# Optimization experiments

Measured on AMD Instinct MI355X. Metric: run time of the kernel, lower is better.

## Reference

```python
import jax, jax.numpy as jnp
import numpy as np

B, S, HID = 2, 2048, 2304
H, KVH, D = 8, 4, 256          # query heads, kv heads, head_dim
N_REP = H // KVH
SCALE = 256.0 ** -0.5          # query_pre_attn_scalar ** -0.5
SOFTCAP = 50.0
ROPE_THETA = 10000.0
NEG = -1e9


def setup_inputs() -> dict:
    key = jax.random.key(0)
    k1, k2, k3, k4, k5 = jax.random.split(key, 5)
    hidden_states = jax.random.normal(k1, (B, S, HID), dtype=jnp.float32)
    # RoPE cos/sin tables, shape [B, S, D]
    inv_freq = 1.0 / (ROPE_THETA ** (jnp.arange(0, D, 2, dtype=jnp.float32) / D))
    pos = jnp.arange(S, dtype=jnp.float32)
    freqs = pos[:, None] * inv_freq[None, :]            # [S, D/2]
    emb = jnp.concatenate([freqs, freqs], axis=-1)      # [S, D]
    cos = jnp.broadcast_to(jnp.cos(emb)[None], (B, S, D))
    sin = jnp.broadcast_to(jnp.sin(emb)[None], (B, S, D))
    # additive causal mask [B, 1, S, S] (sliding_window=4096 > S, so pure causal)
    idx = jnp.arange(S)
    causal = idx[None, :] <= idx[:, None]
    attention_mask = jnp.broadcast_to(
        jnp.where(causal, 0.0, NEG).astype(jnp.float32)[None, None], (B, 1, S, S))
    # projection weights (lecun-normal-ish scale), no bias (attention_bias=False)
    Wq = jax.random.normal(k2, (HID, H * D), dtype=jnp.float32) / np.sqrt(HID)
    Wk = jax.random.normal(k3, (HID, KVH * D), dtype=jnp.float32) / np.sqrt(HID)
    Wv = jax.random.normal(k4, (HID, KVH * D), dtype=jnp.float32) / np.sqrt(HID)
    Wo = jax.random.normal(k5, (H * D, HID), dtype=jnp.float32) / np.sqrt(H * D)
    return {"hidden_states": hidden_states, "cos": cos, "sin": sin,
            "attention_mask": attention_mask,
            "Wq": Wq, "Wk": Wk, "Wv": Wv, "Wo": Wo}


def _rotate_half(x):
    half = x.shape[-1] // 2
    return jnp.concatenate([-x[..., half:], x[..., :half]], axis=-1)


def reference(hidden_states, cos, sin, attention_mask, Wq, Wk, Wv, Wo):
    b, s, _ = hidden_states.shape
    q = (hidden_states @ Wq).reshape(b, s, H, D).transpose(0, 2, 1, 3)    # [B,H,S,D]
    k = (hidden_states @ Wk).reshape(b, s, KVH, D).transpose(0, 2, 1, 3)  # [B,KVH,S,D]
    v = (hidden_states @ Wv).reshape(b, s, KVH, D).transpose(0, 2, 1, 3)
    c = cos[:, None]  # [B,1,S,D] broadcast over heads (unsqueeze_dim=1)
    sn = sin[:, None]
    q = q * c + _rotate_half(q) * sn
    k = k * c + _rotate_half(k) * sn
    # GQA: repeat kv heads (interleave, matching repeat_kv tile+reshape)
    k = jnp.repeat(k, N_REP, axis=1)
    v = jnp.repeat(v, N_REP, axis=1)
    w = jnp.einsum('bhqd,bhkd->bhqk', q, k) * SCALE
    w = jnp.tanh(w / SOFTCAP) * SOFTCAP                  # logit softcapping
    w = w + attention_mask[:, :, :, :s]
    w = jax.nn.softmax(w.astype(jnp.float32), axis=-1).astype(q.dtype)
    out = jnp.einsum('bhqk,bhkd->bhqd', w, v)
    out = out.transpose(0, 2, 1, 3).reshape(b, s, H * D)
    return out @ Wo
```

## Files before the change

### kernel.cpp

```cpp
#include <hip/hip_runtime.h>

typedef unsigned short u16;
typedef __attribute__((ext_vector_type(8))) short short8;
typedef __attribute__((ext_vector_type(4))) float f32x4;

constexpr int B_ = 2;
constexpr int H_ = 8;
constexpr int KVH_ = 4;
constexpr int S_ = 2048;
constexpr int D_ = 256;
constexpr int HID_ = 2304;
constexpr int QKVN_ = 4096;
constexpr int AON_ = 2048;

__device__ __forceinline__ float b2f(u16 u) {
  union { float f; unsigned int i; } x; x.i = ((unsigned int)u) << 16; return x.f;
}
__device__ __forceinline__ u16 f2b(float f) {
  unsigned int x = __float_as_uint(f);
  unsigned int r = (x + 0x7fffu + ((x >> 16) & 1u)) >> 16;
  return (u16)r;
}

__global__ void cast_kernel(const float* __restrict__ in, u16* __restrict__ out) {
  size_t i = ((size_t)blockIdx.x * 256 + threadIdx.x) * 4;
  float4 v = *(const float4*)(in + i);
  unsigned int lo = (unsigned int)f2b(v.x) | ((unsigned int)f2b(v.y) << 16);
  unsigned int hi = (unsigned int)f2b(v.z) | ((unsigned int)f2b(v.w) << 16);
  uint2 o; o.x = lo; o.y = hi;
  *(uint2*)(out + i) = o;
}

__global__ void transpose_cast(const float* __restrict__ src, u16* __restrict__ dst,
                               int R, int C) {
  __shared__ float tile[64][65];
  int r0 = blockIdx.y * 64, c0 = blockIdx.x * 64;
  int t = threadIdx.x;
#pragma unroll
  for (int i = 0; i < 16; ++i) {
    int e = i * 256 + t;
    int r = e >> 6, c = e & 63;
    tile[r][c] = src[(size_t)(r0 + r) * C + (c0 + c)];
  }
  __syncthreads();
#pragma unroll
  for (int i = 0; i < 16; ++i) {
    int e = i * 256 + t;
    int orow = e >> 6, ocol = e & 63;
    dst[(size_t)(c0 + orow) * R + (r0 + ocol)] = f2b(tile[ocol][orow]);
  }
}

template <int OUTF32>
__global__ __launch_bounds__(256, 2) void gemm_bt(
    const u16* __restrict__ A, const u16* __restrict__ B, void* __restrict__ Cp,
    int M, int N, int K) {
  __shared__ u16 As[128 * 32];
  __shared__ u16 Bs[128 * 32];
  int m0 = blockIdx.y * 128, n0 = blockIdx.x * 128;
  int tid = threadIdx.x;
  int lane = tid & 63, wave = tid >> 6;
  int wy = wave >> 1, wx = wave & 1;
  int quad = lane >> 4, l16 = lane & 15;
  f32x4 acc[4][4] = {};
  for (int k0 = 0; k0 < K; k0 += 32) {
#pragma unroll
    for (int i = 0; i < 2; ++i) {
      int chunk = i * 256 + tid;
      int row = chunk >> 2, col = (chunk & 3) << 3;
      __builtin_amdgcn_global_load_lds(
          (const __attribute__((address_space(1))) void*)(A + (size_t)(m0 + row) * K + k0 + col),
          (__attribute__((address_space(3))) void*)(As + chunk * 8), 16, 0, 0);
    }
#pragma unroll
    for (int i = 0; i < 2; ++i) {
      int chunk = i * 256 + tid;
      int row = chunk >> 2, col = (chunk & 3) << 3;
      __builtin_amdgcn_global_load_lds(
          (const __attribute__((address_space(1))) void*)(B + (size_t)(n0 + row) * K + k0 + col),
          (__attribute__((address_space(3))) void*)(Bs + chunk * 8), 16, 0, 0);
    }
    __syncthreads();
    short8 af[4], bf[4];
#pragma unroll
    for (int mi = 0; mi < 4; ++mi)
      af[mi] = *(const short8*)(As + (wy * 64 + mi * 16 + l16) * 32 + quad * 8);
#pragma unroll
    for (int ni = 0; ni < 4; ++ni)
      bf[ni] = *(const short8*)(Bs + (wx * 64 + ni * 16 + l16) * 32 + quad * 8);
#pragma unroll
    for (int mi = 0; mi < 4; ++mi)
#pragma unroll
      for (int ni = 0; ni < 4; ++ni)
        acc[mi][ni] = __builtin_amdgcn_mfma_f32_16x16x32_bf16(af[mi], bf[ni], acc[mi][ni], 0, 0, 0);
    __syncthreads();
  }
#pragma unroll
  for (int mi = 0; mi < 4; ++mi) {
#pragma unroll
    for (int ni = 0; ni < 4; ++ni) {
#pragma unroll
      for (int r = 0; r < 4; ++r) {
        int row = m0 + wy * 64 + mi * 16 + quad * 4 + r;
        int col = n0 + wx * 64 + ni * 16 + l16;
        if (OUTF32)
          ((float*)Cp)[(size_t)row * N + col] = acc[mi][ni][r];
        else
          ((u16*)Cp)[(size_t)row * N + col] = f2b(acc[mi][ni][r]);
      }
    }
  }
}

__global__ void rope_kernel(const u16* __restrict__ qkv, const float* __restrict__ cs,
                            const float* __restrict__ sn, u16* __restrict__ Qr,
                            u16* __restrict__ Kr) {
  int row = blockIdx.x;
  int b = row >> 11, s = row & 2047;
  int d = threadIdx.x;
  const u16* qrow = qkv + (size_t)row * QKVN_;
  float c = cs[(size_t)row * D_ + d];
  float si = sn[(size_t)row * D_ + d];
  int dp = (d < 128) ? d + 128 : d - 128;
  float sgn = (d < 128) ? -1.f : 1.f;
#pragma unroll
  for (int h = 0; h < H_; ++h) {
    float v = b2f(qrow[h * D_ + d]);
    float p = sgn * b2f(qrow[h * D_ + dp]);
    Qr[((size_t)(b * H_ + h) * S_ + s) * D_ + d] = f2b(v * c + p * si);
  }
#pragma unroll
  for (int g = 0; g < KVH_; ++g) {
    float v = b2f(qrow[2048 + g * D_ + d]);
    float p = sgn * b2f(qrow[2048 + g * D_ + dp]);
    Kr[((size_t)(b * KVH_ + g) * S_ + s) * D_ + d] = f2b(v * c + p * si);
  }
}

__global__ void transpose_v(const u16* __restrict__ qkv, u16* __restrict__ Vt) {
  __shared__ u16 tile[64][72];
  int d0 = blockIdx.x * 64, s0 = blockIdx.y * 64, g = blockIdx.z;
  int b = g >> 2, kvh = g & 3;
  int t = threadIdx.x;
#pragma unroll
  for (int i = 0; i < 16; ++i) {
    int e = i * 256 + t;
    int r = e >> 6, c = e & 63;
    tile[r][c] = qkv[(size_t)(b * S_ + s0 + r) * QKVN_ + 3072 + kvh * D_ + d0 + c];
  }
  __syncthreads();
#pragma unroll
  for (int i = 0; i < 16; ++i) {
    int e = i * 256 + t;
    int orow = e >> 6, ocol = e & 63;
    Vt[((size_t)g * D_ + d0 + orow) * S_ + s0 + ocol] = tile[ocol][orow];
  }
}

__global__ __launch_bounds__(256, 2) void attn_kernel(
    const u16* __restrict__ Qr, const u16* __restrict__ Kr, const u16* __restrict__ Vt,
    u16* __restrict__ Ao) {
  __shared__ u16 Ks[2][32 * 256];
  __shared__ u16 Vs[2][32 * 256];
  __shared__ u16 Ps[4][16 * 40];
  int b = blockIdx.z;
  int qt = (b == 0) ? (31 - blockIdx.x) : blockIdx.x;
  int h = blockIdx.y;
  int kvh = h >> 1;
  int tid = threadIdx.x, wave = tid >> 6, lane = tid & 63;
  int quad = lane >> 4, l16 = lane & 15;
  int q0 = qt * 64;
  const u16* Qbase = Qr + ((size_t)(b * H_ + h) * S_ + q0 + wave * 16 + l16) * D_;
  short8 qf[8];
#pragma unroll
  for (int kk = 0; kk < 8; ++kk)
    qf[kk] = *(const short8*)(Qbase + kk * 32 + quad * 8);
  const u16* Kbase = Kr + (size_t)(b * KVH_ + kvh) * S_ * D_;
  const u16* Vbase = Vt + (size_t)(b * KVH_ + kvh) * D_ * S_;
  int ksrc_s[4], ksrc_c[4], vsrc_d[4], vsrc_s[4];
#pragma unroll
  for (int i = 0; i < 4; ++i) {
    int p = i * 256 + tid;
    ksrc_s[i] = p >> 5;
    ksrc_c[i] = (p & 31) ^ ((p >> 5) & 7);
    vsrc_d[i] = p >> 2;
    vsrc_s[i] = (p & 3) ^ ((p >> 3) & 3);
  }
  float lp[4] = {0.f, 0.f, 0.f, 0.f};
  f32x4 o_acc[16] = {};
  int nkt = 2 * qt + 2;

#define STAGE(KT, BUF)                                                                   \
  {                                                                                      \
    int k0s = (KT) * 32;                                                                 \
    _Pragma("unroll") for (int i = 0; i < 4; ++i) {                                      \
      int p = i * 256 + tid;                                                             \
      __builtin_amdgcn_global_load_lds(                                                  \
          (const __attribute__((address_space(1))) void*)(Kbase +                        \
              (size_t)(k0s + ksrc_s[i]) * D_ + ksrc_c[i] * 8),                           \
          (__attribute__((address_space(3))) void*)(&Ks[BUF][0] + p * 8), 16, 0, 0);     \
    }                                                                                    \
    _Pragma("unroll") for (int i = 0; i < 4; ++i) {                                      \
      int p = i * 256 + tid;                                                             \
      __builtin_amdgcn_global_load_lds(                                                  \
          (const __attribute__((address_space(1))) void*)(Vbase +                        \
              (size_t)vsrc_d[i] * S_ + k0s + vsrc_s[i] * 8),                             \
          (__attribute__((address_space(3))) void*)(&Vs[BUF][0] + p * 8), 16, 0, 0);     \
    }                                                                                    \
  }

  STAGE(0, 0);
  __syncthreads();
  for (int kt = 0; kt < nkt; ++kt) {
    int k0 = kt * 32;
    int cur = kt & 1;
    if (kt + 1 < nkt) STAGE(kt + 1, cur ^ 1);
    f32x4 sacc[2] = {};
#pragma unroll
    for (int n = 0; n < 2; ++n) {
      int srow = n * 16 + l16;
      const u16* kb = &Ks[cur][0] + srow * 256;
      int sw = l16 & 7;
#pragma unroll
      for (int kk = 0; kk < 8; ++kk) {
        int phys = (kk * 4 + quad) ^ sw;
        short8 bfr = *(const short8*)(kb + phys * 8);
        sacc[n] = __builtin_amdgcn_mfma_f32_16x16x32_bf16(qf[kk], bfr, sacc[n], 0, 0, 0);
      }
    }
    bool full = (k0 + 31 <= q0 + wave * 16);
#pragma unroll
    for (int n = 0; n < 2; ++n) {
      int key = k0 + n * 16 + l16;
#pragma unroll
      for (int r = 0; r < 4; ++r) {
        float E = __expf(sacc[n][r] * 0.0025f);
        float ee = __expf(-100.0f * __frcp_rn(E + 1.0f));
        if (!full) {
          int qq = q0 + wave * 16 + quad * 4 + r;
          ee = (key <= qq) ? ee : 0.0f;
        }
        lp[r] += ee;
        Ps[wave][(quad * 4 + r) * 40 + n * 16 + l16] = f2b(ee);
      }
    }
    short8 pa = *(const short8*)(&Ps[wave][l16 * 40 + quad * 8]);
#pragma unroll
    for (int dt = 0; dt < 16; ++dt) {
      int d = dt * 16 + l16;
      int phys = quad ^ ((d >> 1) & 3);
      short8 vb = *(const short8*)(&Vs[cur][0] + d * 32 + phys * 8);
      o_acc[dt] = __builtin_amdgcn_mfma_f32_16x16x32_bf16(pa, vb, o_acc[dt], 0, 0, 0);
    }
    __syncthreads();
  }
#undef STAGE
#pragma unroll
  for (int off = 1; off < 16; off <<= 1)
#pragma unroll
    for (int r = 0; r < 4; ++r)
      lp[r] += __shfl_xor(lp[r], off, 64);
#pragma unroll
  for (int r = 0; r < 4; ++r) lp[r] = 1.0f / lp[r];
#pragma unroll
  for (int dt = 0; dt < 16; ++dt)
#pragma unroll
    for (int r = 0; r < 4; ++r) {
      int row = b * S_ + q0 + wave * 16 + quad * 4 + r;
      int col = h * D_ + dt * 16 + l16;
      Ao[(size_t)row * AON_ + col] = f2b(o_acc[dt][r] * lp[r]);
    }
}

extern "C" void kernel_launch(void* const* d_in, const int* in_sizes, int n_in,
                              void* d_out, int out_size, void* d_ws, size_t ws_size,
                              hipStream_t stream) {
  const float* hidden = (const float*)d_in[0];
  const float* cosp = (const float*)d_in[1];
  const float* sinp = (const float*)d_in[2];
  const float* Wq = (const float*)d_in[4];
  const float* Wk = (const float*)d_in[5];
  const float* Wv = (const float*)d_in[6];
  const float* Wo = (const float*)d_in[7];

  u16* hs  = (u16*)d_ws;
  u16* WT  = hs  + (size_t)4096 * HID_;
  u16* WoT = WT  + (size_t)4096 * HID_;
  u16* qkv = WoT + (size_t)HID_ * AON_;
  u16* Qr  = qkv + (size_t)4096 * QKVN_;
  u16* Kr  = Qr  + (size_t)B_ * H_ * S_ * D_;
  u16* Vt  = Kr  + (size_t)B_ * KVH_ * S_ * D_;
  u16* Ao  = Vt  + (size_t)B_ * KVH_ * S_ * D_;

  cast_kernel<<<9216, 256, 0, stream>>>(hidden, hs);
  transpose_cast<<<dim3(32, 36), 256, 0, stream>>>(Wq, WT, HID_, 2048);
  transpose_cast<<<dim3(16, 36), 256, 0, stream>>>(Wk, WT + (size_t)2048 * HID_, HID_, 1024);
  transpose_cast<<<dim3(16, 36), 256, 0, stream>>>(Wv, WT + (size_t)3072 * HID_, HID_, 1024);
  transpose_cast<<<dim3(36, 32), 256, 0, stream>>>(Wo, WoT, 2048, HID_);
  gemm_bt<0><<<dim3(32, 32), 256, 0, stream>>>(hs, WT, qkv, 4096, QKVN_, HID_);
  rope_kernel<<<4096, 256, 0, stream>>>(qkv, cosp, sinp, Qr, Kr);
  transpose_v<<<dim3(4, 32, 8), 256, 0, stream>>>(qkv, Vt);
  attn_kernel<<<dim3(32, 8, 2), 256, 0, stream>>>(Qr, Kr, Vt, Ao);
  gemm_bt<1><<<dim3(18, 32), 256, 0, stream>>>(Ao, WoT, d_out, 4096, HID_, 2048);
}
```

Measured before the change: 441.2 us.

## Split attention KV range across two blocks with paired causal tiles and combine

Attention now pairs a short and a long causal query tile per block, one from each batch, and splits each tile's key range into two halves handled by separate blocks. The blocks write unnormalised fp32 partial outputs and row sums, and a new combine kernel adds them and normalises to bf16. This balances work across blocks and removes the causal tail imbalance, at the cost of extra fp32 global traffic and one more kernel launch. Separately, the four weight transpose launches are merged into one launch.

```diff
diff --git a/kernel.cpp b/kernel.cpp
--- a/kernel.cpp
+++ b/kernel.cpp
@@ -31,10 +31,19 @@
   *(uint2*)(out + i) = o;
 }
 
-__global__ void transpose_cast(const float* __restrict__ src, u16* __restrict__ dst,
-                               int R, int C) {
+__global__ void transpose_cast_all(const float* __restrict__ s0, const float* __restrict__ s1,
+                                   const float* __restrict__ s2, const float* __restrict__ s3,
+                                   u16* __restrict__ d0, u16* __restrict__ d1,
+                                   u16* __restrict__ d2, u16* __restrict__ d3) {
   __shared__ float tile[64][65];
+  int which = blockIdx.z;
+  const float* src; u16* dst; int R, C;
+  if (which == 0)      { src = s0; dst = d0; R = 2304; C = 2048; }
+  else if (which == 1) { src = s1; dst = d1; R = 2304; C = 1024; }
+  else if (which == 2) { src = s2; dst = d2; R = 2304; C = 1024; }
+  else                 { src = s3; dst = d3; R = 2048; C = 2304; }
   int r0 = blockIdx.y * 64, c0 = blockIdx.x * 64;
+  if (r0 >= R || c0 >= C) return;
   int t = threadIdx.x;
 #pragma unroll
   for (int i = 0; i < 16; ++i) {
@@ -159,24 +168,18 @@
 
 __global__ __launch_bounds__(256, 2) void attn_kernel(
     const u16* __restrict__ Qr, const u16* __restrict__ Kr, const u16* __restrict__ Vt,
-    u16* __restrict__ Ao) {
+    float* __restrict__ Op0, float* __restrict__ Op1,
+    float* __restrict__ Lp0, float* __restrict__ Lp1) {
   __shared__ u16 Ks[2][32 * 256];
   __shared__ u16 Vs[2][32 * 256];
   __shared__ u16 Ps[4][16 * 40];
-  int b = blockIdx.z;
-  int qt = (b == 0) ? (31 - blockIdx.x) : blockIdx.x;
+  int u = blockIdx.x >> 1, sp = blockIdx.x & 1;
   int h = blockIdx.y;
   int kvh = h >> 1;
   int tid = threadIdx.x, wave = tid >> 6, lane = tid & 63;
   int quad = lane >> 4, l16 = lane & 15;
-  int q0 = qt * 64;
-  const u16* Qbase = Qr + ((size_t)(b * H_ + h) * S_ + q0 + wave * 16 + l16) * D_;
-  short8 qf[8];
-#pragma unroll
-  for (int kk = 0; kk < 8; ++kk)
-    qf[kk] = *(const short8*)(Qbase + kk * 32 + quad * 8);
-  const u16* Kbase = Kr + (size_t)(b * KVH_ + kvh) * S_ * D_;
-  const u16* Vbase = Vt + (size_t)(b * KVH_ + kvh) * D_ * S_;
+  float* Op = sp ? Op1 : Op0;
+  float* Lp = sp ? Lp1 : Lp0;
   int ksrc_s[4], ksrc_c[4], vsrc_d[4], vsrc_s[4];
 #pragma unroll
   for (int i = 0; i < 4; ++i) {
@@ -186,90 +189,125 @@
     vsrc_d[i] = p >> 2;
     vsrc_s[i] = (p & 3) ^ ((p >> 3) & 3);
   }
-  float lp[4] = {0.f, 0.f, 0.f, 0.f};
-  f32x4 o_acc[16] = {};
-  int nkt = 2 * qt + 2;
+
+  for (int part = 0; part < 2; ++part) {
+    int b = part;
+    int qt = (part == 0) ? u : (31 - u);
+    int q0 = qt * 64;
+    int beg = sp ? (qt + 1) : 0;
+    int end = sp ? (2 * qt + 2) : (qt + 1);
+    const u16* Qbase = Qr + ((size_t)(b * H_ + h) * S_ + q0 + wave * 16 + l16) * D_;
+    short8 qf[8];
+#pragma unroll
+    for (int kk = 0; kk < 8; ++kk)
+      qf[kk] = *(const short8*)(Qbase + kk * 32 + quad * 8);
+    const u16* Kbase = Kr + (size_t)(b * KVH_ + kvh) * S_ * D_;
+    const u16* Vbase = Vt + (size_t)(b * KVH_ + kvh) * D_ * S_;
+    float lp[4] = {0.f, 0.f, 0.f, 0.f};
+    f32x4 o_acc[16] = {};
 
 #define STAGE(KT, BUF)                                                                   \
-  {                                                                                      \
-    int k0s = (KT) * 32;                                                                 \
-    _Pragma("unroll") for (int i = 0; i < 4; ++i) {                                      \
-      int p = i * 256 + tid;                                                             \
-      __builtin_amdgcn_global_load_lds(                                                  \
-          (const __attribute__((address_space(1))) void*)(Kbase +                        \
-              (size_t)(k0s + ksrc_s[i]) * D_ + ksrc_c[i] * 8),                           \
-          (__attribute__((address_space(3))) void*)(&Ks[BUF][0] + p * 8), 16, 0, 0);     \
-    }                                                                                    \
-    _Pragma("unroll") for (int i = 0; i < 4; ++i) {                                      \
-      int p = i * 256 + tid;                                                             \
-      __builtin_amdgcn_global_load_lds(                                                  \
-          (const __attribute__((address_space(1))) void*)(Vbase +                        \
-              (size_t)vsrc_d[i] * S_ + k0s + vsrc_s[i] * 8),                             \
-          (__attribute__((address_space(3))) void*)(&Vs[BUF][0] + p * 8), 16, 0, 0);     \
-    }                                                                                    \
-  }
-
-  STAGE(0, 0);
-  __syncthreads();
-  for (int kt = 0; kt < nkt; ++kt) {
-    int k0 = kt * 32;
-    int cur = kt & 1;
-    if (kt + 1 < nkt) STAGE(kt + 1, cur ^ 1);
-    f32x4 sacc[2] = {};
-#pragma unroll
-    for (int n = 0; n < 2; ++n) {
-      int srow = n * 16 + l16;
-      const u16* kb = &Ks[cur][0] + srow * 256;
-      int sw = l16 & 7;
-#pragma unroll
-      for (int kk = 0; kk < 8; ++kk) {
-        int phys = (kk * 4 + quad) ^ sw;
-        short8 bfr = *(const short8*)(kb + phys * 8);
-        sacc[n] = __builtin_amdgcn_mfma_f32_16x16x32_bf16(qf[kk], bfr, sacc[n], 0, 0, 0);
-      }
-    }
-    bool full = (k0 + 31 <= q0 + wave * 16);
-#pragma unroll
-    for (int n = 0; n < 2; ++n) {
-      int key = k0 + n * 16 + l16;
+    {                                                                                    \
+      int k0s = (KT) * 32;                                                               \
+      _Pragma("unroll") for (int i = 0; i < 4; ++i) {                                    \
+        int p = i * 256 + tid;                                                           \
+        __builtin_amdgcn_global_load_lds(                                                \
+            (const __attribute__((address_space(1))) void*)(Kbase +                      \
+                (size_t)(k0s + ksrc_s[i]) * D_ + ksrc_c[i] * 8),                         \
+            (__attribute__((address_space(3))) void*)(&Ks[BUF][0] + p * 8), 16, 0, 0);   \
+      }                                                                                  \
+      _Pragma("unroll") for (int i = 0; i < 4; ++i) {                                    \
+        int p = i * 256 + tid;                                                           \
+        __builtin_amdgcn_global_load_lds(                                                \
+            (const __attribute__((address_space(1))) void*)(Vbase +                      \
+                (size_t)vsrc_d[i] * S_ + k0s + vsrc_s[i] * 8),                           \
+            (__attribute__((address_space(3))) void*)(&Vs[BUF][0] + p * 8), 16, 0, 0);   \
+      }                                                                                  \
+    }
+
+    STAGE(beg, 0);
+    __syncthreads();
+    for (int kt = beg; kt < end; ++kt) {
+      int k0 = kt * 32;
+      int cur = (kt - beg) & 1;
+      if (kt + 1 < end) STAGE(kt + 1, cur ^ 1);
+      f32x4 sacc[2] = {};
+#pragma unroll
+      for (int n = 0; n < 2; ++n) {
+        int srow = n * 16 + l16;
+        const u16* kb = &Ks[cur][0] + srow * 256;
+        int sw = l16 & 7;
+#pragma unroll
+        for (int kk = 0; kk < 8; ++kk) {
+          int phys = (kk * 4 + quad) ^ sw;
+          short8 bfr = *(const short8*)(kb + phys * 8);
+          sacc[n] = __builtin_amdgcn_mfma_f32_16x16x32_bf16(qf[kk], bfr, sacc[n], 0, 0, 0);
+        }
+      }
+      bool full = (k0 + 31 <= q0 + wave * 16);
+#pragma unroll
+      for (int n = 0; n < 2; ++n) {
+        int key = k0 + n * 16 + l16;
+#pragma unroll
+        for (int r = 0; r < 4; ++r) {
+          float E = __expf(sacc[n][r] * 0.0025f);
+          float ee = __expf(-100.0f * __frcp_rn(E + 1.0f));
+          if (!full) {
+            int qq = q0 + wave * 16 + quad * 4 + r;
+            ee = (key <= qq) ? ee : 0.0f;
+          }
+          lp[r] += ee;
+          Ps[wave][(quad * 4 + r) * 40 + n * 16 + l16] = f2b(ee);
+        }
+      }
+      short8 pa = *(const short8*)(&Ps[wave][l16 * 40 + quad * 8]);
+#pragma unroll
+      for (int dt = 0; dt < 16; ++dt) {
+        int d = dt * 16 + l16;
+        int phys = quad ^ ((d >> 1) & 3);
+        short8 vb = *(const short8*)(&Vs[cur][0] + d * 32 + phys * 8);
+        o_acc[dt] = __builtin_amdgcn_mfma_f32_16x16x32_bf16(pa, vb, o_acc[dt], 0, 0, 0);
+      }
+      __syncthreads();
+    }
+#undef STAGE
+#pragma unroll
+    for (int off = 1; off < 16; off <<= 1)
+#pragma unroll
+      for (int r = 0; r < 4; ++r)
+        lp[r] += __shfl_xor(lp[r], off, 64);
+    if (l16 == 0) {
+#pragma unroll
+      for (int r = 0; r < 4; ++r)
+        Lp[((size_t)(b * H_ + h)) * S_ + q0 + wave * 16 + quad * 4 + r] = lp[r];
+    }
+#pragma unroll
+    for (int dt = 0; dt < 16; ++dt)
 #pragma unroll
       for (int r = 0; r < 4; ++r) {
-        float E = __expf(sacc[n][r] * 0.0025f);
-        float ee = __expf(-100.0f * __frcp_rn(E + 1.0f));
-        if (!full) {
-          int qq = q0 + wave * 16 + quad * 4 + r;
-          ee = (key <= qq) ? ee : 0.0f;
-        }
-        lp[r] += ee;
-        Ps[wave][(quad * 4 + r) * 40 + n * 16 + l16] = f2b(ee);
-      }
-    }
-    short8 pa = *(const short8*)(&Ps[wave][l16 * 40 + quad * 8]);
-#pragma unroll
-    for (int dt = 0; dt < 16; ++dt) {
-      int d = dt * 16 + l16;
-      int phys = quad ^ ((d >> 1) & 3);
-      short8 vb = *(const short8*)(&Vs[cur][0] + d * 32 + phys * 8);
-      o_acc[dt] = __builtin_amdgcn_mfma_f32_16x16x32_bf16(pa, vb, o_acc[dt], 0, 0, 0);
-    }
-    __syncthreads();
-  }
-#undef STAGE
-#pragma unroll
-  for (int off = 1; off < 16; off <<= 1)
-#pragma unroll
-    for (int r = 0; r < 4; ++r)
-      lp[r] += __shfl_xor(lp[r], off, 64);
-#pragma unroll
-  for (int r = 0; r < 4; ++r) lp[r] = 1.0f / lp[r];
-#pragma unroll
-  for (int dt = 0; dt < 16; ++dt)
-#pragma unroll
-    for (int r = 0; r < 4; ++r) {
-      int row = b * S_ + q0 + wave * 16 + quad * 4 + r;
-      int col = h * D_ + dt * 16 + l16;
-      Ao[(size_t)row * AON_ + col] = f2b(o_acc[dt][r] * lp[r]);
-    }
+        int row = b * S_ + q0 + wave * 16 + quad * 4 + r;
+        int col = h * D_ + dt * 16 + l16;
+        Op[(size_t)row * AON_ + col] = o_acc[dt][r];
+      }
+  }
+}
+
+__global__ void combine_kernel(const float* __restrict__ Op0, const float* __restrict__ Op1,
+                               const float* __restrict__ Lp0, const float* __restrict__ Lp1,
+                               u16* __restrict__ Ao) {
+  size_t idx = (size_t)blockIdx.x * 256 + threadIdx.x;
+  size_t row = idx >> 9;
+  int c4 = ((int)idx & 511) * 4;
+  const float4 a = *(const float4*)(Op0 + row * AON_ + c4);
+  const float4 b4 = *(const float4*)(Op1 + row * AON_ + c4);
+  int b = (int)(row >> 11), s = (int)row & 2047;
+  int h = c4 >> 8;
+  size_t li = ((size_t)(b * H_ + h)) * S_ + s;
+  float inv = 1.0f / (Lp0[li] + Lp1[li]);
+  unsigned int lo = (unsigned int)f2b((a.x + b4.x) * inv) | ((unsigned int)f2b((a.y + b4.y) * inv) << 16);
+  unsigned int hi = (unsigned int)f2b((a.z + b4.z) * inv) | ((unsigned int)f2b((a.w + b4.w) * inv) << 16);
+  uint2 o; o.x = lo; o.y = hi;
+  *(uint2*)(Ao + row * AON_ + c4) = o;
 }
 
 extern "C" void kernel_launch(void* const* d_in, const int* in_sizes, int n_in,
@@ -291,15 +329,18 @@
   u16* Kr  = Qr  + (size_t)B_ * H_ * S_ * D_;
   u16* Vt  = Kr  + (size_t)B_ * KVH_ * S_ * D_;
   u16* Ao  = Vt  + (size_t)B_ * KVH_ * S_ * D_;
+  float* Lp0 = (float*)(Ao + (size_t)4096 * AON_);
+  float* Lp1 = Lp0 + (size_t)B_ * H_ * S_;
+  float* Op0 = (float*)hs;
+  float* Op1 = (float*)qkv;
 
   cast_kernel<<<9216, 256, 0, stream>>>(hidden, hs);
-  transpose_cast<<<dim3(32, 36), 256, 0, stream>>>(Wq, WT, HID_, 2048);
-  transpose_cast<<<dim3(16, 36), 256, 0, stream>>>(Wk, WT + (size_t)2048 * HID_, HID_, 1024);
-  transpose_cast<<<dim3(16, 36), 256, 0, stream>>>(Wv, WT + (size_t)3072 * HID_, HID_, 1024);
-  transpose_cast<<<dim3(36, 32), 256, 0, stream>>>(Wo, WoT, 2048, HID_);
+  transpose_cast_all<<<dim3(36, 36, 4), 256, 0, stream>>>(
+      Wq, Wk, Wv, Wo, WT, WT + (size_t)2048 * HID_, WT + (size_t)3072 * HID_, WoT);
   gemm_bt<0><<<dim3(32, 32), 256, 0, stream>>>(hs, WT, qkv, 4096, QKVN_, HID_);
   rope_kernel<<<4096, 256, 0, stream>>>(qkv, cosp, sinp, Qr, Kr);
   transpose_v<<<dim3(4, 32, 8), 256, 0, stream>>>(qkv, Vt);
-  attn_kernel<<<dim3(32, 8, 2), 256, 0, stream>>>(Qr, Kr, Vt, Ao);
+  attn_kernel<<<dim3(64, 8), 256, 0, stream>>>(Qr, Kr, Vt, Op0, Op1, Lp0, Lp1);
+  combine_kernel<<<16384, 256, 0, stream>>>(Op0, Op1, Lp0, Lp1, Ao);
   gemm_bt<1><<<dim3(18, 32), 256, 0, stream>>>(Ao, WoT, d_out, 4096, HID_, 2048);
 }
```

Result: faster. 427.6 us (-3.1%).
